# Kernel optimization log

Measured on AMD Instinct MI355X. Metric: run time of the kernel, lower is better.

## Reference

```python
import jax, jax.numpy as jnp
import numpy as np

_INF = 1e9  # large finite 'infinity' for squared distances (max real sq-dist ~ 3*47^2)


def _minplus_last(f):
    """Exact 1D squared Euclidean distance transform along the last axis:
    g[x] = min_j f[j] + (x - j)^2 (brute-force min-plus, fully vectorized)."""
    n = f.shape[-1]
    i = jnp.arange(n)
    d2 = ((i[:, None] - i[None, :]) ** 2).astype(f.dtype)  # (n_out, n_in)
    return jnp.min(f[..., None, :] + d2, axis=-1)


def _edt(src):
    """Exact Euclidean distance to the nearest True voxel of `src` over the last
    3 (spatial) axes. Equivalent to scipy.ndimage.distance_transform_edt(~src)
    (distance to nearest zero of ~src). Separable squared-distance passes."""
    f = jnp.where(src, 0.0, _INF).astype(jnp.float32)
    for ax in (-3, -2, -1):
        f = jnp.moveaxis(_minplus_last(jnp.moveaxis(f, ax, -1)), -1, ax)
    return jnp.sqrt(f)


def _signed_distance_maps(onehot):
    """onehot: (B, C, D, H, W) in {0,1}. Returns SDF = posdis - negdis per (b,c),
    zeroed where the class is absent in that batch element (matches torch code)."""
    pos = onehot.astype(bool)
    stacked = jnp.stack([pos, ~pos], axis=0)          # (2, B, C, D, H, W)
    dists = _edt(stacked)                              # exact EDT for both masks
    posdis, negdis = dists[0], dists[1]
    has_pos = pos.any(axis=(-3, -2, -1))               # (B, C)
    sdf = jnp.where(has_pos[..., None, None, None], posdis - negdis, 0.0)
    return sdf


def setup_inputs() -> dict:
    key = jax.random.key(0)
    k1, k2 = jax.random.split(key)
    B, C, D, H, W = 2, 4, 48, 48, 48
    pred = jax.random.normal(k1, (B, C, D, H, W), dtype=jnp.float32)
    target = jax.random.randint(k2, (B, D, H, W), 0, C, dtype=jnp.int64)
    return {"pred": pred, "target": target}


def reference(pred, target):
    num_classes = pred.shape[1]
    # one-hot encode target: (B, C, D, H, W)
    onehot = (target[:, None] == jnp.arange(num_classes)[None, :, None, None, None])
    onehot = onehot.astype(jnp.float32)
    pred_softmax = jax.nn.softmax(pred, axis=1)
    sdf = _signed_distance_maps(onehot)                # no-grad quantity
    return jnp.mean(jnp.abs(pred_softmax * sdf))
```

## Files before the change

### kernel.cpp

```cpp
#include <hip/hip_runtime.h>
#include <hip/hip_bf16.h>


#define SPATIAL 110592
#define NB 2
#define NC 4
#define NLINE 48
#define SLABP 49

__global__ __launch_bounds__(192) void edt_wh_kernel(const int* __restrict__ target,
                                                     float* __restrict__ F,
                                                     float* __restrict__ out) {
    __shared__ float slab[NLINE * SLABP];
    __shared__ int tsh[NLINE * NLINE];
    int blk = blockIdx.x;
    int vol = blk / NLINE, d = blk - vol * NLINE;
    int mask = vol >> 3;
    int b = (vol >> 2) & 1, c = vol & 3;
    int tid = threadIdx.x;
    if (blk == 0 && tid == 0) *out = 0.0f;

    const int* tslab = target + (b * NLINE + d) * (NLINE * NLINE);
    for (int idx = tid; idx < NLINE * NLINE; idx += 192) tsh[idx] = tslab[idx];
    __syncthreads();

    if (tid < NLINE) {
        int h = tid;
        int n = 64;
        for (int w = 0; w < NLINE; ++w) {
            int t = tsh[h * NLINE + w];
            bool set = mask ? (t != c) : (t == c);
            n = set ? 0 : n + 1;
            slab[h * SLABP + w] = (float)n;
        }
        n = 64;
        for (int w = NLINE - 1; w >= 0; --w) {
            int t = tsh[h * NLINE + w];
            bool set = mask ? (t != c) : (t == c);
            n = set ? 0 : n + 1;
            float m = fminf(slab[h * SLABP + w], (float)n);
            slab[h * SLABP + w] = (m >= 48.0f) ? 1e9f : m * m;
        }
    }
    __syncthreads();

    {
        int w = tid >> 2, cx = (tid & 3) * 12;
        float m[12];
#pragma unroll
        for (int k = 0; k < 12; ++k) m[k] = 1e30f;
        float dj = (float)cx;
        for (int j = 0; j < NLINE; j += 2) {
            float f0 = slab[j * SLABP + w];
            float f1 = slab[(j + 1) * SLABP + w];
            float a0 = fmaf(dj, dj, f0);
            float dj1 = dj - 1.0f;
            float a1 = fmaf(dj1, dj1, f1);
#pragma unroll
            for (int k = 0; k < 12; ++k) {
                float tk = (float)(2 * k);
                m[k] = fminf(fminf(m[k], fmaf(tk, dj, a0)), fmaf(tk, dj1, a1));
            }
            dj -= 2.0f;
        }
        __syncthreads();
#pragma unroll
        for (int k = 0; k < 12; ++k)
            slab[(cx + k) * SLABP + w] = m[k] + (float)(k * k);
        __syncthreads();
    }

    float* fvol = F + (long)vol * SPATIAL + (long)d * (NLINE * NLINE);
    for (int idx = tid; idx < NLINE * NLINE; idx += 192) {
        int h = idx / NLINE, ww = idx - h * NLINE;
        fvol[idx] = slab[h * SLABP + ww];
    }
}

__global__ __launch_bounds__(192) void edt_d_reduce_kernel(const float* __restrict__ pred,
                                                           const float* __restrict__ F,
                                                           float* __restrict__ out) {
    __shared__ float slabP[NLINE * SLABP];
    __shared__ float slabN[NLINE * SLABP];
    int blk = blockIdx.x;
    int half = blk & 1;
    int rest = blk >> 1;
    int bc = rest / NLINE, h = rest - bc * NLINE;
    int b = bc >> 2, c = bc & 3;
    int tid = threadIdx.x;

    const float* fp = F + (long)bc * SPATIAL;
    const float* fn = F + (long)(8 + bc) * SPATIAL;
    for (int idx = tid; idx < NLINE * NLINE; idx += 192) {
        int dd = idx / NLINE, ww = idx - dd * NLINE;
        long g = (long)dd * (NLINE * NLINE) + h * NLINE + ww;
        slabP[dd * SLABP + ww] = fp[g];
        slabN[dd * SLABP + ww] = fn[g];
    }
    __syncthreads();

    int w = tid >> 2;
    int cx = half * 24 + (tid & 3) * 6;
    float mP[6], mN[6];
#pragma unroll
    for (int k = 0; k < 6; ++k) { mP[k] = 1e30f; mN[k] = 1e30f; }
    float dj = (float)cx;
    for (int j = 0; j < NLINE; j += 2) {
        float fp0 = slabP[j * SLABP + w];
        float fn0 = slabN[j * SLABP + w];
        float fp1 = slabP[(j + 1) * SLABP + w];
        float fn1 = slabN[(j + 1) * SLABP + w];
        float dj1 = dj - 1.0f;
        float aP0 = fmaf(dj, dj, fp0),  aP1 = fmaf(dj1, dj1, fp1);
        float aN0 = fmaf(dj, dj, fn0),  aN1 = fmaf(dj1, dj1, fn1);
#pragma unroll
        for (int k = 0; k < 6; ++k) {
            float tk = (float)(2 * k);
            mP[k] = fminf(fminf(mP[k], fmaf(tk, dj, aP0)), fmaf(tk, dj1, aP1));
            mN[k] = fminf(fminf(mN[k], fmaf(tk, dj, aN0)), fmaf(tk, dj1, aN1));
        }
        dj -= 2.0f;
    }

    float acc = 0.0f;
    long pbase = (long)b * NC * SPATIAL + (long)h * NLINE + w;
#pragma unroll
    for (int k = 0; k < 6; ++k) {
        int d = cx + k;
        float psq = mP[k] + (float)(k * k);
        float nsq = mN[k] + (float)(k * k);
        float sdf = (psq > 1e8f) ? 0.0f : (sqrtf(psq) - sqrtf(nsq));
        long base = pbase + (long)d * (NLINE * NLINE);
        float p0 = pred[base];
        float p1 = pred[base + SPATIAL];
        float p2 = pred[base + 2 * SPATIAL];
        float p3 = pred[base + 3 * SPATIAL];
        float mx = fmaxf(fmaxf(p0, p1), fmaxf(p2, p3));
        float e0 = __expf(p0 - mx), e1 = __expf(p1 - mx);
        float e2 = __expf(p2 - mx), e3 = __expf(p3 - mx);
        float sum = e0 + e1 + e2 + e3;
        float ec = (c == 0) ? e0 : (c == 1) ? e1 : (c == 2) ? e2 : e3;
        acc += (ec / sum) * fabsf(sdf);
    }

#pragma unroll
    for (int o = 32; o > 0; o >>= 1) acc += __shfl_down(acc, o, 64);
    __shared__ float wpart[3];
    int lane = tid & 63, wid = tid >> 6;
    if (lane == 0) wpart[wid] = acc;
    __syncthreads();
    if (tid == 0) {
        float v = wpart[0] + wpart[1] + wpart[2];
        atomicAdd(out, v * (1.0f / (float)(NB * NC * SPATIAL)));
    }
}

extern "C" void kernel_launch(void* const* d_in, const int* in_sizes, int n_in,
                              void* d_out, int out_size, void* d_ws, size_t ws_size,
                              hipStream_t stream) {
    const float* pred = (const float*)d_in[0];
    const int* target = (const int*)d_in[1];
    float* out = (float*)d_out;
    float* F = (float*)d_ws;

    edt_wh_kernel<<<2 * NB * NC * NLINE, 192, 0, stream>>>(target, F, out);
    edt_d_reduce_kernel<<<2 * NB * NC * NLINE, 192, 0, stream>>>(pred, F, out);
}
```

Baseline: 91.16 us.

## Compute W-axis distances with wave ballots and vectorize slab copies with float4

```diff
diff --git a/kernel.cpp b/kernel.cpp
--- a/kernel.cpp
+++ b/kernel.cpp
@@ -6,13 +6,13 @@
 #define NB 2
 #define NC 4
 #define NLINE 48
-#define SLABP 49
+#define SLABP 52
+#define MAGIC_INF 1e9f
 
 __global__ __launch_bounds__(192) void edt_wh_kernel(const int* __restrict__ target,
                                                      float* __restrict__ F,
                                                      float* __restrict__ out) {
     __shared__ float slab[NLINE * SLABP];
-    __shared__ int tsh[NLINE * NLINE];
     int blk = blockIdx.x;
     int vol = blk / NLINE, d = blk - vol * NLINE;
     int mask = vol >> 3;
@@ -20,26 +20,24 @@
     int tid = threadIdx.x;
     if (blk == 0 && tid == 0) *out = 0.0f;
 
-    const int* tslab = target + (b * NLINE + d) * (NLINE * NLINE);
-    for (int idx = tid; idx < NLINE * NLINE; idx += 192) tsh[idx] = tslab[idx];
-    __syncthreads();
-
-    if (tid < NLINE) {
-        int h = tid;
-        int n = 64;
-        for (int w = 0; w < NLINE; ++w) {
-            int t = tsh[h * NLINE + w];
-            bool set = mask ? (t != c) : (t == c);
-            n = set ? 0 : n + 1;
-            slab[h * SLABP + w] = (float)n;
-        }
-        n = 64;
-        for (int w = NLINE - 1; w >= 0; --w) {
-            int t = tsh[h * NLINE + w];
-            bool set = mask ? (t != c) : (t == c);
-            n = set ? 0 : n + 1;
-            float m = fminf(slab[h * SLABP + w], (float)n);
-            slab[h * SLABP + w] = (m >= 48.0f) ? 1e9f : m * m;
+    {
+        int wid = tid >> 6, lane = tid & 63;
+        const int* tbase = target + ((b * NLINE + d) * NLINE) * NLINE;
+#pragma unroll 4
+        for (int r = 0; r < 16; ++r) {
+            int h = wid * 16 + r;
+            int t = (lane < NLINE) ? tbase[h * NLINE + lane] : -1;
+            bool inset = mask ? (lane < NLINE && t != c) : (t == c);
+            unsigned long long m = __ballot(inset);
+            if (lane < NLINE) {
+                unsigned long long low = m & (~0ull >> (63 - lane));
+                unsigned long long high = m >> lane;
+                int left  = low  ? (lane - (63 - __builtin_clzll(low))) : 64;
+                int right = high ? __builtin_ctzll(high) : 64;
+                int dmin = min(left, right);
+                slab[h * SLABP + lane] = (dmin >= NLINE) ? MAGIC_INF
+                                                         : (float)(dmin * dmin);
+            }
         }
     }
     __syncthreads();
@@ -71,9 +69,10 @@
     }
 
     float* fvol = F + (long)vol * SPATIAL + (long)d * (NLINE * NLINE);
-    for (int idx = tid; idx < NLINE * NLINE; idx += 192) {
-        int h = idx / NLINE, ww = idx - h * NLINE;
-        fvol[idx] = slab[h * SLABP + ww];
+    for (int q = tid; q < (NLINE * NLINE) / 4; q += 192) {
+        int h = q / 12, col4 = (q - h * 12) * 4;
+        float4 v = *(const float4*)&slab[h * SLABP + col4];
+        *(float4*)&fvol[h * NLINE + col4] = v;
     }
 }
 
@@ -89,13 +88,15 @@
     int b = bc >> 2, c = bc & 3;
     int tid = threadIdx.x;
 
-    const float* fp = F + (long)bc * SPATIAL;
-    const float* fn = F + (long)(8 + bc) * SPATIAL;
-    for (int idx = tid; idx < NLINE * NLINE; idx += 192) {
-        int dd = idx / NLINE, ww = idx - dd * NLINE;
-        long g = (long)dd * (NLINE * NLINE) + h * NLINE + ww;
-        slabP[dd * SLABP + ww] = fp[g];
-        slabN[dd * SLABP + ww] = fn[g];
+    const float* fp = F + (long)bc * SPATIAL + (long)h * NLINE;
+    const float* fn = F + (long)(8 + bc) * SPATIAL + (long)h * NLINE;
+    for (int q = tid; q < (NLINE * NLINE) / 4; q += 192) {
+        int dd = q / 12, col4 = (q - dd * 12) * 4;
+        long g = (long)dd * (NLINE * NLINE) + col4;
+        float4 vp = *(const float4*)&fp[g];
+        float4 vn = *(const float4*)&fn[g];
+        *(float4*)&slabP[dd * SLABP + col4] = vp;
+        *(float4*)&slabN[dd * SLABP + col4] = vn;
     }
     __syncthreads();
 
```

After: 88.24 us. 1.03x faster.
